# Kernel tuning notes

Measured on AMD Instinct MI355X. Metric: run time of the kernel, lower is better.

Reference implementation:

```python
import jax, jax.numpy as jnp
import numpy as np

B, T, D, H = 512, 200, 128, 128


def setup_inputs() -> dict:
    key = jax.random.key(0)
    ks = jax.random.split(key, 16)
    r = lambda k, shp, s=0.05: jax.random.normal(k, shp, dtype=jnp.float32) * s
    F = 3 * D + H  # concat([item_eb, his_sum, item_eb*his_sum, final_state2])
    return {
        "item_eb": jax.random.normal(ks[0], (B, D), dtype=jnp.float32),
        "item_his_eb": jax.random.normal(ks[1], (B, T, D), dtype=jnp.float32),
        "Wg1": r(ks[2], (D + H, 2 * H)), "bg1": jnp.ones((2 * H,), jnp.float32),
        "Wc1": r(ks[3], (D + H, H)), "bc1": jnp.zeros((H,), jnp.float32),
        "att_w1": r(ks[4], (4 * H, 80)), "att_b1": jnp.zeros((80,), jnp.float32),
        "att_w2": r(ks[5], (80, 40)), "att_b2": jnp.zeros((40,), jnp.float32),
        "att_w3": r(ks[6], (40, 1)), "att_b3": jnp.zeros((1,), jnp.float32),
        "Wg2": r(ks[7], (2 * H, 2 * H)), "bg2": jnp.ones((2 * H,), jnp.float32),
        "Wc2": r(ks[8], (2 * H, H)), "bc2": jnp.zeros((H,), jnp.float32),
        "fc1_w": r(ks[9], (F, 200)), "fc1_b": jnp.zeros((200,), jnp.float32),
        "alpha1": jnp.full((200,), 0.25, jnp.float32),
        "fc2_w": r(ks[10], (200, 80)), "fc2_b": jnp.zeros((80,), jnp.float32),
        "alpha2": jnp.full((80,), 0.25, jnp.float32),
        "fc3_w": r(ks[11], (80, 2)), "fc3_b": jnp.zeros((2,), jnp.float32),
        "seq_len": jax.random.randint(ks[12], (B,), 1, T + 1).astype(jnp.int32),
    }


def _gru_scan(x_btd, Wg, bg, Wc, bc, seq_len, att=None):
    """GRU (TF GRUCell math) or AUGRU if att [B,T] is given.
    Honors sequence_length semantics of tf dynamic_rnn: state copied through,
    outputs zeroed past each row's length."""
    Bx, Tx, _ = x_btd.shape
    Hh = Wc.shape[1]
    xs = jnp.swapaxes(x_btd, 0, 1)  # [T,B,Din]
    ts = jnp.arange(Tx)
    a_ts = jnp.swapaxes(att, 0, 1) if att is not None else jnp.zeros((Tx, Bx), x_btd.dtype)
    h0 = jnp.zeros((Bx, Hh), x_btd.dtype)

    def step(h, xat):
        x, a, t = xat
        gates = jax.nn.sigmoid(jnp.concatenate([x, h], axis=-1) @ Wg + bg)
        rg, u = jnp.split(gates, 2, axis=-1)
        c = jnp.tanh(jnp.concatenate([x, rg * h], axis=-1) @ Wc + bc)
        if att is not None:  # VecAttGRUCell: u = (1 - att_score) * u
            u = (1.0 - a[:, None]) * u
        hn = u * h + (1.0 - u) * c
        valid = (t < seq_len)[:, None]
        hn = jnp.where(valid, hn, h)
        out = jnp.where(valid, hn, jnp.zeros_like(hn))
        return hn, out

    hT, outs = jax.lax.scan(step, h0, (xs, a_ts, ts))
    return jnp.swapaxes(outs, 0, 1), hT  # [B,T,H], [B,H]


def _forward(item_eb, item_his_eb, Wg1, bg1, Wc1, bc1, att_w1, att_b1, att_w2, att_b2,
             att_w3, att_b3, Wg2, bg2, Wc2, bc2, fc1_w, fc1_b, alpha1, fc2_w, fc2_b,
             alpha2, fc3_w, fc3_b, seq_len):
    Bx, Tx, Dx = item_his_eb.shape
    mask = jnp.arange(Tx)[None, :] < seq_len[:, None]  # [B,T] bool
    # rnn_1: plain GRU over history embeddings
    rnn1, _ = _gru_scan(item_his_eb, Wg1, bg1, Wc1, bc1, seq_len)
    # din_fcn_attention: concat trick + 3-layer scorer + masked softmax
    q = jnp.broadcast_to(item_eb[:, None, :], rnn1.shape)
    din_all = jnp.concatenate([q, rnn1, q - rnn1, q * rnn1], axis=-1)  # [B,T,4H]
    h1 = jax.nn.sigmoid(din_all @ att_w1 + att_b1)
    h2 = jax.nn.sigmoid(h1 @ att_w2 + att_b2)
    scores = (h2 @ att_w3 + att_b3)[..., 0]  # [B,T]
    NEG_INF = jnp.float32(-(2.0 ** 32) + 1.0)  # DIEN padding value
    scores = jnp.where(mask, scores, NEG_INF)
    alphas = jax.nn.softmax(scores, axis=-1)  # [B,T]
    # rnn_2: AUGRU (VecAttGRUCell) gated by attention scores; take final state
    _, final_state2 = _gru_scan(rnn1, Wg2, bg2, Wc2, bc2, seq_len, att=alphas)
    # fcn head on concatenated features
    his_sum = jnp.sum(item_his_eb * mask[..., None].astype(item_his_eb.dtype), axis=1)
    feat = jnp.concatenate([item_eb, his_sum, item_eb * his_sum, final_state2], axis=-1)
    prelu = lambda x, a: jnp.maximum(x, 0.0) + a * jnp.minimum(x, 0.0)
    z = prelu(feat @ fc1_w + fc1_b, alpha1)
    z = prelu(z @ fc2_w + fc2_b, alpha2)
    logits = z @ fc3_w + fc3_b  # [B,2]
    return jax.nn.softmax(logits, axis=-1)


def reference(item_eb, item_his_eb, Wg1, bg1, Wc1, bc1, att_w1, att_b1, att_w2, att_b2,
              att_w3, att_b3, Wg2, bg2, Wc2, bc2, fc1_w, fc1_b, alpha1, fc2_w, fc2_b,
              alpha2, fc3_w, fc3_b, seq_len):
    return _forward(item_eb, item_his_eb, Wg1, bg1, Wc1, bc1, att_w1, att_b1, att_w2,
                    att_b2, att_w3, att_b3, Wg2, bg2, Wc2, bc2, fc1_w, fc1_b, alpha1,
                    fc2_w, fc2_b, alpha2, fc3_w, fc3_b, seq_len)
```

## Files before the change

kernel.cpp:

```cpp
#include <hip/hip_runtime.h>
#include <hip/hip_bf16.h>


typedef __attribute__((ext_vector_type(8))) short bf16x8;
typedef __attribute__((ext_vector_type(4))) float f32x4;
typedef _Float16 f16x2 __attribute__((ext_vector_type(2)));

#define NC 4
#define TC 50
#define CROWS 25600
#define CSH 3276800

static __device__ __forceinline__ unsigned short f2bf(float f) {
  union { __hip_bfloat16 h; unsigned short u; } v;
  v.h = __float2bfloat16(f);
  return v.u;
}
static __device__ __forceinline__ float bf2f(unsigned short u) {
  union { __hip_bfloat16 h; unsigned short u; } v;
  v.u = u;
  return __bfloat162float(v.h);
}
static __device__ __forceinline__ unsigned short f2h(float f) {
  union { _Float16 h; unsigned short u; } v;
  v.h = (_Float16)f;
  return v.u;
}
static __device__ __forceinline__ float h2f(unsigned short u) {
  union { unsigned short u; _Float16 h; } v;
  v.u = u;
  return (float)v.h;
}
static __device__ __forceinline__ unsigned int pkf16(float a, float b) {
  union { f16x2 v; unsigned int u; } c;
  c.v = (f16x2){(_Float16)a, (_Float16)b};
  return c.u;
}
static __device__ __forceinline__ void dot2a(float& acc, unsigned int w, unsigned int h) {
  asm volatile("v_dot2_f32_f16 %0, %1, %2, %0" : "+v"(acc) : "v"(w), "v"(h));
}
static __device__ __forceinline__ unsigned short gld_u16(const unsigned short* p) {
  return *(const __attribute__((address_space(1))) unsigned short*)p;
}
static __device__ __forceinline__ float gld_f32(const float* p) {
  return *(const __attribute__((address_space(1))) float*)p;
}
static __device__ __forceinline__ void gst_u16(unsigned short* p, unsigned short v) {
  *(__attribute__((address_space(1))) unsigned short*)p = v;
}
static __device__ __forceinline__ void gst_u32(unsigned int* p, unsigned int v) {
  *(__attribute__((address_space(1))) unsigned int*)p = v;
}
static __device__ __forceinline__ void gst_f32(float* p, float v) {
  *(__attribute__((address_space(1))) float*)p = v;
}
static __device__ __forceinline__ void gbar() {
  __builtin_amdgcn_sched_barrier(0);
  asm volatile("s_waitcnt lgkmcnt(0)" ::: "memory");
  __builtin_amdgcn_s_barrier();
  __builtin_amdgcn_sched_barrier(0);
}

__global__ __launch_bounds__(256) void prep_weights(
    const float* __restrict__ item_eb,
    const float* __restrict__ Wg1, const float* __restrict__ Wc1,
    const float* __restrict__ Wg2, const float* __restrict__ Wc2,
    const float* __restrict__ aw1, const float* __restrict__ aw2,
    const float* __restrict__ aw3,
    const float* __restrict__ bg1, const float* __restrict__ bc1,
    const float* __restrict__ bg2, const float* __restrict__ bc2,
    const float* __restrict__ ab1, const float* __restrict__ ab2,
    unsigned short* __restrict__ W1xT, unsigned short* __restrict__ W2xT,
    unsigned short* __restrict__ AW1T, unsigned short* __restrict__ AW2T,
    float* __restrict__ b384_1, float* __restrict__ b384_2,
    float* __restrict__ bA1, float* __restrict__ bA2,
    unsigned int* __restrict__ WgP1, unsigned int* __restrict__ WcP1,
    unsigned int* __restrict__ WgP2, unsigned int* __restrict__ WcP2,
    float* __restrict__ w3p, unsigned short* __restrict__ Xq,
    float* __restrict__ hstate)
{
  int e = blockIdx.x * 256 + threadIdx.x;
  if (e < 49152) {
    int n = e >> 7, k = e & 127;
    float v1 = (n < 256) ? Wg1[k * 256 + n] : Wc1[k * 128 + (n - 256)];
    float v2 = (n < 256) ? Wg2[k * 256 + n] : Wc2[k * 128 + (n - 256)];
    W1xT[e] = f2bf(v1);
    W2xT[e] = f2bf(v2);
  }
  if (e < 65536) {
    int n = e >> 9, k = e & 511;
    AW1T[e] = f2bf(n < 80 ? aw1[k * 80 + n] : 0.f);
    Xq[e] = f2bf(item_eb[e]);
    hstate[e] = 0.f;
  }
  if (e < 16384) {
    int n = e >> 7, k = e & 127;
    AW2T[e] = f2bf((n < 40 && k < 80) ? aw2[k * 40 + n] : 0.f);
  }
  if (e < 16384) {
    int i = e >> 8, tt = e & 255;
    int row = 128 + 2 * i;
    WgP1[e] = pkf16(Wg1[row * 256 + tt], Wg1[(row + 1) * 256 + tt]);
    WgP2[e] = pkf16(Wg2[row * 256 + tt], Wg2[(row + 1) * 256 + tt]);
  }
  if (e < 8192) {
    int i = e >> 8, tt = e & 255;
    int jc = tt >> 1, half = tt & 1;
    int row = 128 + half * 64 + 2 * i;
    WcP1[e] = pkf16(Wc1[row * 128 + jc], Wc1[(row + 1) * 128 + jc]);
    WcP2[e] = pkf16(Wc2[row * 128 + jc], Wc2[(row + 1) * 128 + jc]);
  }
  if (e < 384) {
    b384_1[e] = (e < 256) ? bg1[e] : bc1[e - 256];
    b384_2[e] = (e < 256) ? bg2[e] : bc2[e - 256];
  }
  if (e < 128) {
    bA1[e] = (e < 80) ? ab1[e] : 0.f;
    bA2[e] = (e < 40) ? ab2[e] : 0.f;
    w3p[e] = (e < 40) ? aw3[e] : 0.f;
  }
}

__global__ __launch_bounds__(256) void cast_his_t(const float4* __restrict__ in4,
                                                  ushort4* __restrict__ out4)
{
  int i = blockIdx.x * 256 + threadIdx.x;
  float4 v = in4[i];
  int d4 = (i & 31) << 2;
  int bt = i >> 5;
  int tt = bt % 200, bb = bt / 200;
  out4[(((size_t)tt * 512 + bb) * 128 + d4) >> 2] =
      make_ushort4(f2bf(v.x), f2bf(v.y), f2bf(v.z), f2bf(v.w));
}

struct GemmP {
  const unsigned short* A;
  const unsigned short* B;
  const float* bias;
  unsigned short* out;
  float* scores;
  const float* w3p;
  const float* b3;
  const unsigned short* Xq;
  const unsigned short* rnn1;
  long rowbase;
  int K, ldc, mtiles, tbase;
};

static __device__ __forceinline__ uint4 bfop(uint4 q, uint4 r, bool mul) {
  unsigned short* qs = (unsigned short*)&q;
  unsigned short* rs = (unsigned short*)&r;
  uint4 o;
  unsigned short* os = (unsigned short*)&o;
#pragma unroll
  for (int i = 0; i < 8; i++) {
    float a = bf2f(qs[i]), b = bf2f(rs[i]);
    os[i] = f2bf(mul ? a * b : a - b);
  }
  return o;
}

template <int SRC, int EPI>
__device__ __forceinline__ void gemm_body(const GemmP& P, int tile, char* smem) {
  uint4* AsB = (uint4*)smem;
  uint4* BsB = AsB + 1024;
  const int tid = threadIdx.x;
  const int w = tid >> 6, l = tid & 63;
  const int mb = tile % P.mtiles, nb = tile / P.mtiles;
  const long mBase = (long)mb * 128;
  const int nBase = nb * 128;

  f32x4 acc[2][8];
#pragma unroll
  for (int m = 0; m < 2; m++)
#pragma unroll
    for (int n = 0; n < 8; n++) acc[m][n] = 0.f;

  const int srow = (tid >> 3) & 31;
  const int scc = l & 7;
  const int KK = SRC ? 512 : P.K;

  for (int kb = 0; kb < KK; kb += 64) {
#pragma unroll
    for (int p = 0; p < 4; p++) {
      int row = p * 32 + srow;
      long grow = mBase + row;
      uint4 va;
      if (SRC == 0) {
        va = *(const uint4*)(P.A + (size_t)grow * KK + kb + scc * 8);
      } else {
        int seg = kb >> 7;
        int c0 = (kb & 127) + scc * 8;
        int b = (int)(grow & 511);
        if (seg == 0) {
          va = *(const uint4*)(P.Xq + b * 128 + c0);
        } else if (seg == 1) {
          va = *(const uint4*)(P.rnn1 + (size_t)(P.rowbase + grow) * 128 + c0);
        } else {
          uint4 vq = *(const uint4*)(P.Xq + b * 128 + c0);
          uint4 vr = *(const uint4*)(P.rnn1 + (size_t)(P.rowbase + grow) * 128 + c0);
          va = bfop(vq, vr, seg == 3);
        }
      }
      uint4 vb = *(const uint4*)(P.B + (size_t)(nBase + row) * KK + kb + scc * 8);
      AsB[row * 8 + (scc ^ (row & 7))] = va;
      BsB[row * 8 + (scc ^ (row & 7))] = vb;
    }
    __syncthreads();
#pragma unroll
    for (int ks = 0; ks < 2; ks++) {
      int ccr = ks * 4 + (l >> 4);
      int r0 = w * 32 + (l & 15);
      int r1 = r0 + 16;
      bf16x8 a0 = *(const bf16x8*)&AsB[r0 * 8 + (ccr ^ (r0 & 7))];
      bf16x8 a1 = *(const bf16x8*)&AsB[r1 * 8 + (ccr ^ (r1 & 7))];
#pragma unroll
      for (int n = 0; n < 8; n++) {
        int rb = n * 16 + (l & 15);
        bf16x8 bn = *(const bf16x8*)&BsB[rb * 8 + (ccr ^ (rb & 7))];
        acc[0][n] = __builtin_amdgcn_mfma_f32_16x16x32_bf16(a0, bn, acc[0][n], 0, 0, 0);
        acc[1][n] = __builtin_amdgcn_mfma_f32_16x16x32_bf16(a1, bn, acc[1][n], 0, 0, 0);
      }
    }
    __syncthreads();
  }

  const int lcol = l & 15, lrow4 = (l >> 4) * 4;
  if (EPI == 2) {
    float sp[2][4] = {{0.f, 0.f, 0.f, 0.f}, {0.f, 0.f, 0.f, 0.f}};
#pragma unroll
    for (int n = 0; n < 8; n++) {
      int gcol = n * 16 + lcol;
      float bb = P.bias[gcol];
      float w3 = P.w3p[gcol];
#pragma unroll
      for (int m = 0; m < 2; m++)
#pragma unroll
        for (int i = 0; i < 4; i++) {
          float v = acc[m][n][i] + bb;
          sp[m][i] += w3 / (1.f + __expf(-v));
        }
    }
#pragma unroll
    for (int msk = 1; msk < 16; msk <<= 1)
#pragma unroll
      for (int m = 0; m < 2; m++)
#pragma unroll
        for (int i = 0; i < 4; i++) sp[m][i] += __shfl_xor(sp[m][i], msk);
    float b3v = P.b3[0];
    if (lcol == 0) {
#pragma unroll
      for (int m = 0; m < 2; m++)
#pragma unroll
        for (int i = 0; i < 4; i++) {
          long grow = mBase + w * 32 + m * 16 + lrow4 + i;
          int b = (int)(grow & 511);
          int tp = (int)(grow >> 9) + P.tbase;
          P.scores[b * 200 + tp] = sp[m][i] + b3v;
        }
    }
  } else {
#pragma unroll
    for (int n = 0; n < 8; n++) {
      int gcol = nBase + n * 16 + lcol;
      float bb = P.bias[gcol];
#pragma unroll
      for (int m = 0; m < 2; m++)
#pragma unroll
        for (int i = 0; i < 4; i++) {
          long grow = mBase + w * 32 + m * 16 + lrow4 + i;
          float v = acc[m][n][i] + bb;
          if (EPI == 0) P.out[grow * P.ldc + gcol] = f2h(v);
          else          P.out[grow * P.ldc + gcol] = f2bf(1.f / (1.f + __expf(-v)));
        }
    }
  }
}

struct GruP {
  const unsigned short* xproj;
  const unsigned int* WgP;
  const unsigned int* WcP;
  const int* seqlen;
  const float* alphas;
  unsigned short* outbf;
  float* hstate;
  int tbase;
};

template <int AUGRU>
static __device__ __forceinline__ void gstep(
    const GruP& P, int r, int t, int jc, int half, int len, int ts, int tsn,
    const unsigned int (&wg)[64], const unsigned int (&wc)[32],
    float* hF, float* uF, unsigned short* hH, unsigned short* rgH,
    unsigned short& gX, unsigned short& cX, float& alX)
{
  const unsigned short* xp = P.xproj;
  const size_t RS = (size_t)512 * 384;
  const size_t base = (size_t)r * 384;
  float xg = h2f(gX), xc = h2f(cX), alv = alX;
  size_t off = (size_t)tsn * RS + base;
  gX = gld_u16(xp + off + t);
  cX = gld_u16(xp + off + 256 + jc);
  if (AUGRU) alX = gld_f32(P.alphas + r * 200 + P.tbase + tsn);

  float a0 = 0.f, a1 = 0.f, a2 = 0.f, a3 = 0.f;
  const uint4* h4 = (const uint4*)hH;
#pragma unroll
  for (int q = 0; q < 4; q++) {
    uint4 h0 = h4[q * 4 + 0];
    uint4 h1 = h4[q * 4 + 1];
    uint4 h2 = h4[q * 4 + 2];
    uint4 h3 = h4[q * 4 + 3];
    dot2a(a0, wg[q * 16 + 0], h0.x);  dot2a(a1, wg[q * 16 + 1], h0.y);
    dot2a(a2, wg[q * 16 + 2], h0.z);  dot2a(a3, wg[q * 16 + 3], h0.w);
    dot2a(a0, wg[q * 16 + 4], h1.x);  dot2a(a1, wg[q * 16 + 5], h1.y);
    dot2a(a2, wg[q * 16 + 6], h1.z);  dot2a(a3, wg[q * 16 + 7], h1.w);
    dot2a(a0, wg[q * 16 + 8], h2.x);  dot2a(a1, wg[q * 16 + 9], h2.y);
    dot2a(a2, wg[q * 16 + 10], h2.z); dot2a(a3, wg[q * 16 + 11], h2.w);
    dot2a(a0, wg[q * 16 + 12], h3.x); dot2a(a1, wg[q * 16 + 13], h3.y);
    dot2a(a2, wg[q * 16 + 14], h3.z); dot2a(a3, wg[q * 16 + 15], h3.w);
  }
  float a = (a0 + a1) + (a2 + a3) + xg;
  float g = 1.f / (1.f + __expf(-a));
  if (t < 128) rgH[t] = f2h(g * hF[t]);
  else         uF[t - 128] = g;
  gbar();

  float c0 = 0.f, c1 = 0.f;
  const uint4* rp = (const uint4*)rgH + half * 8;
#pragma unroll
  for (int q = 0; q < 8; q++) {
    uint4 rq = rp[q];
    dot2a(c0, wc[q * 4 + 0], rq.x);
    dot2a(c1, wc[q * 4 + 1], rq.y);
    dot2a(c0, wc[q * 4 + 2], rq.z);
    dot2a(c1, wc[q * 4 + 3], rq.w);
  }
  float c = c0 + c1;
  c += __shfl_xor(c, 1);
  c += xc;
  c = fminf(fmaxf(c, -15.f), 15.f);
  float e2 = __expf(2.f * c);
  c = 1.f - 2.f / (e2 + 1.f);
  float u = uF[jc];
  if (AUGRU) u *= (1.f - alv);
  float h = hF[jc];
  float hn = u * h + (1.f - u) * c;
  bool valid = (P.tbase + ts) < len;
  hn = valid ? hn : h;
  if (!half) {
    hF[jc] = hn;
    hH[jc] = f2h(hn);
    if (!AUGRU)
      gst_u16(P.outbf + ((size_t)(P.tbase + ts) * 512 + r) * 128 + jc,
              valid ? f2bf(hn) : (unsigned short)0);
  }
  gbar();
}

template <int AUGRU>
__device__ void gru_body(const GruP& P, int r, char* smem) {
  float* hF = (float*)smem;
  float* uF = hF + 128;
  unsigned short* hH = (unsigned short*)(uF + 128);
  unsigned short* rgH = hH + 128;
  const int t = threadIdx.x;
  const int jc = t >> 1, half = t & 1;
  const int len = P.seqlen[r];
  int nsteps = len - P.tbase;
  if (nsteps > TC) nsteps = TC;

  if (nsteps <= 0) {
    if (!AUGRU && t < 64) {
      for (int s = 0; s < TC; s++)
        gst_u32((unsigned int*)(P.outbf + ((size_t)(P.tbase + s) * 512 + r) * 128) + t, 0u);
    }
    return;
  }
  __builtin_amdgcn_s_setprio(1);

  unsigned int wg[64], wc[32];
#pragma unroll
  for (int i = 0; i < 64; i++) wg[i] = P.WgP[i * 256 + t];
#pragma unroll
  for (int i = 0; i < 32; i++) wc[i] = P.WcP[i * 256 + t];

  if (t < 128) {
    float h = gld_f32(P.hstate + r * 128 + t);
    hF[t] = h;
    hH[t] = f2h(h);
  }
  gbar();

  const unsigned short* xp = P.xproj;
  const size_t RS = (size_t)512 * 384;
  const size_t base = (size_t)r * 384;
  unsigned short gE = gld_u16(xp + base + t), cE = gld_u16(xp + base + 256 + jc);
  int s1 = nsteps > 1 ? 1 : 0;
  unsigned short gO = gld_u16(xp + s1 * RS + base + t);
  unsigned short cO = gld_u16(xp + s1 * RS + base + 256 + jc);
  float alE = AUGRU ? gld_f32(P.alphas + r * 200 + P.tbase) : 0.f;
  float alO = AUGRU ? gld_f32(P.alphas + r * 200 + P.tbase + s1) : 0.f;

  int rsteps = (nsteps + 1) & ~1;
  for (int ts = 0; ts < rsteps; ts += 2) {
    int tn0 = (ts + 2 < nsteps) ? ts + 2 : nsteps - 1;
    int tn1 = (ts + 3 < nsteps) ? ts + 3 : nsteps - 1;
    gstep<AUGRU>(P, r, t, jc, half, len, ts,     tn0, wg, wc, hF, uF, hH, rgH, gE, cE, alE);
    gstep<AUGRU>(P, r, t, jc, half, len, ts + 1, tn1, wg, wc, hF, uF, hH, rgH, gO, cO, alO);
  }

  if (t < 128) gst_f32(P.hstate + r * 128 + t, hF[t]);
  if (!AUGRU && t < 64) {
    for (int s = rsteps; s < TC; s++)
      gst_u32((unsigned int*)(P.outbf + ((size_t)(P.tbase + s) * 512 + r) * 128) + t, 0u);
  }
}

__device__ void hsum_body(const float* __restrict__ his, float* __restrict__ hs,
                          const int* __restrict__ seqlen, int b, char* smem) {
  float* sm = (float*)smem;
  int t = threadIdx.x;
  int len = seqlen[b];
  int col = t & 127, hf = t >> 7;
  float s = 0.f;
  for (int ts = hf; ts < len; ts += 2) s += his[((size_t)b * 200 + ts) * 128 + col];
  sm[t] = s;
  __syncthreads();
  if (t < 128) hs[b * 128 + t] = sm[t] + sm[t + 128];
}

template <int AUG, int GRU, int S1, int E1, int S2, int E2, int S3, int E3, int HS>
__global__ __launch_bounds__(256) void fatk(GruP gp, GemmP p1, int c1,
                                            GemmP p2, int c2, GemmP p3,
                                            const float* hisp, float* hsp)
{
  extern __shared__ char smem[];
  int id = blockIdx.x;
  if constexpr (GRU) {
    if (id < 512) { gru_body<AUG>(gp, id, smem); return; }
    id -= 512;
  }
  if constexpr (HS) {
    if (id < 512) { hsum_body(hisp, hsp, gp.seqlen, id, smem); return; }
    id -= 512;
  }
  if constexpr (S1 >= 0) {
    if (id < c1) { gemm_body<S1, E1>(p1, id, smem); return; }
    id -= c1;
  }
  if constexpr (S2 >= 0) {
    if (id < c2) { gemm_body<S2, E2>(p2, id, smem); return; }
    id -= c2;
  }
  if constexpr (S3 >= 0) gemm_body<S3, E3>(p3, id, smem);
}

__global__ __launch_bounds__(256) void mask_softmax(
    const float* __restrict__ scores, const int* __restrict__ seqlen,
    float* __restrict__ alphas, float* __restrict__ hstate)
{
  int b = blockIdx.x, t = threadIdx.x;
  __shared__ float red[256];
  if (t < 128) hstate[b * 128 + t] = 0.f;
  int len = seqlen[b];
  float s = (t < 200 && t < len) ? scores[b * 200 + t] : -1e30f;
  red[t] = s;
  __syncthreads();
  for (int o = 128; o > 0; o >>= 1) {
    if (t < o) red[t] = fmaxf(red[t], red[t + o]);
    __syncthreads();
  }
  float m = red[0];
  __syncthreads();
  float e = (t < 200 && t < len) ? __expf(s - m) : 0.f;
  red[t] = e;
  __syncthreads();
  for (int o = 128; o > 0; o >>= 1) {
    if (t < o) red[t] += red[t + o];
    __syncthreads();
  }
  float denom = red[0];
  if (t < 200) alphas[b * 200 + t] = e / denom;
}

__global__ __launch_bounds__(256) void head_kernel(
    const float* __restrict__ item_eb, const float* __restrict__ hs,
    const float* __restrict__ hstate,
    const float* __restrict__ w1, const float* __restrict__ b1, const float* __restrict__ a1,
    const float* __restrict__ w2, const float* __restrict__ b2, const float* __restrict__ a2,
    const float* __restrict__ w3, const float* __restrict__ b3,
    float* __restrict__ out)
{
  int b = blockIdx.x, t = threadIdx.x;
  __shared__ float frow[512];
  __shared__ float z1[200];
  __shared__ float z2[80];
  if (t < 128) {
    float sv = hs[b * 128 + t];
    float q = item_eb[b * 128 + t];
    frow[t] = q;
    frow[128 + t] = sv;
    frow[256 + t] = q * sv;
    frow[384 + t] = hstate[b * 128 + t];
  }
  __syncthreads();
  if (t < 200) {
    float acc = b1[t];
#pragma unroll 8
    for (int k = 0; k < 512; k++) acc += frow[k] * w1[k * 200 + t];
    z1[t] = acc > 0.f ? acc : a1[t] * acc;
  }
  __syncthreads();
  if (t < 80) {
    float acc = b2[t];
#pragma unroll 8
    for (int k = 0; k < 200; k++) acc += z1[k] * w2[k * 80 + t];
    z2[t] = acc > 0.f ? acc : a2[t] * acc;
  }
  __syncthreads();
  if (t == 0) {
    float l0 = b3[0], l1 = b3[1];
    for (int k = 0; k < 80; k++) {
      float z = z2[k];
      l0 += z * w3[k * 2];
      l1 += z * w3[k * 2 + 1];
    }
    float m = fmaxf(l0, l1);
    float e0 = __expf(l0 - m), e1 = __expf(l1 - m);
    out[b * 2 + 0] = e0 / (e0 + e1);
    out[b * 2 + 1] = e1 / (e0 + e1);
  }
}

extern "C" void kernel_launch(void* const* d_in, const int* in_sizes, int n_in,
                              void* d_out, int out_size, void* d_ws, size_t ws_size,
                              hipStream_t stream)
{
  const float* item_eb = (const float*)d_in[0];
  const float* his     = (const float*)d_in[1];
  const float* Wg1     = (const float*)d_in[2];
  const float* bg1     = (const float*)d_in[3];
  const float* Wc1     = (const float*)d_in[4];
  const float* bc1     = (const float*)d_in[5];
  const float* aw1     = (const float*)d_in[6];
  const float* ab1     = (const float*)d_in[7];
  const float* aw2     = (const float*)d_in[8];
  const float* ab2     = (const float*)d_in[9];
  const float* aw3     = (const float*)d_in[10];
  const float* ab3     = (const float*)d_in[11];
  const float* Wg2     = (const float*)d_in[12];
  const float* bg2     = (const float*)d_in[13];
  const float* Wc2     = (const float*)d_in[14];
  const float* bc2     = (const float*)d_in[15];
  const float* fc1w    = (const float*)d_in[16];
  const float* fc1b    = (const float*)d_in[17];
  const float* al1     = (const float*)d_in[18];
  const float* fc2w    = (const float*)d_in[19];
  const float* fc2b    = (const float*)d_in[20];
  const float* al2     = (const float*)d_in[21];
  const float* fc3w    = (const float*)d_in[22];
  const float* fc3b    = (const float*)d_in[23];
  const int*   seqlen  = (const int*)d_in[24];

  char* ws = (char*)d_ws;
  unsigned short* XhA    = (unsigned short*)(ws + 0L);
  unsigned short* xpA    = (unsigned short*)(ws + 26214400L);
  unsigned short* xpB    = (unsigned short*)(ws + 45875200L);
  unsigned short* rnn1   = (unsigned short*)(ws + 65536000L);
  float*          scores = (float*)(ws + 91750400L);
  float*          alphas = (float*)(ws + 92160000L);
  float*          hstate = (float*)(ws + 92569600L);
  unsigned int*   WgP1   = (unsigned int*)(ws + 92831744L);
  unsigned int*   WcP1   = (unsigned int*)(ws + 92897280L);
  unsigned int*   WgP2   = (unsigned int*)(ws + 92930048L);
  unsigned int*   WcP2   = (unsigned int*)(ws + 92995584L);
  unsigned short* W1xT   = (unsigned short*)(ws + 93028352L);
  unsigned short* W2xT   = (unsigned short*)(ws + 93126656L);
  unsigned short* AW1T   = (unsigned short*)(ws + 93224960L);
  unsigned short* AW2T   = (unsigned short*)(ws + 93356032L);
  float*          b384_1 = (float*)(ws + 93388800L);
  float*          b384_2 = (float*)(ws + 93390336L);
  float*          bA1    = (float*)(ws + 93391872L);
  float*          bA2    = (float*)(ws + 93392384L);
  float*          w3p    = (float*)(ws + 93392896L);
  unsigned short* Xq     = (unsigned short*)(ws + 93393408L);
  float*          hs     = scores;

  unsigned short* h1[NC] = {XhA, XhA + CSH, XhA + 2 * CSH, XhA + 3 * CSH};

  const int SM = 32768;
  GruP gz{}; GemmP dz{};
  gz.seqlen = seqlen;

  auto mkGru = [&](int c, int aug) {
    GruP g;
    g.xproj = (c & 1) ? xpB : xpA;
    g.WgP = aug ? WgP2 : WgP1; g.WcP = aug ? WcP2 : WcP1;
    g.seqlen = seqlen; g.alphas = alphas;
    g.outbf = aug ? nullptr : rnn1; g.hstate = hstate; g.tbase = c * TC;
    return g;
  };
  auto mkXp = [&](const unsigned short* A, const float* bias, unsigned short* outp) {
    GemmP p{}; p.A = A; p.B = (bias == b384_1) ? W1xT : W2xT; p.bias = bias;
    p.out = outp; p.K = 128; p.ldc = 384; p.mtiles = 200; return p;
  };
  auto mkAtt1 = [&](int c) {
    GemmP p{}; p.B = AW1T; p.bias = bA1; p.out = h1[c];
    p.Xq = Xq; p.rnn1 = rnn1; p.rowbase = (long)c * CROWS;
    p.K = 512; p.ldc = 128; p.mtiles = 200; return p;
  };
  auto mkAtt2 = [&](int c) {
    GemmP p{}; p.A = h1[c]; p.B = AW2T; p.bias = bA2;
    p.scores = scores; p.w3p = w3p; p.b3 = ab3;
    p.K = 128; p.ldc = 128; p.mtiles = 200; p.tbase = c * TC; return p;
  };

  prep_weights<<<256, 256, 0, stream>>>(item_eb, Wg1, Wc1, Wg2, Wc2, aw1, aw2, aw3,
                                        bg1, bc1, bg2, bc2, ab1, ab2,
                                        W1xT, W2xT, AW1T, AW2T, b384_1, b384_2, bA1, bA2,
                                        WgP1, WcP1, WgP2, WcP2, w3p, Xq, hstate);
  cast_his_t<<<12800, 256, 0, stream>>>((const float4*)his, (ushort4*)XhA);

  fatk<0,0, 0,0, -1,0, -1,0, 0><<<600, 256, SM, stream>>>(
      gz, mkXp(XhA, b384_1, xpA), 600, dz, 0, dz, nullptr, nullptr);
  fatk<0,1, 0,0, -1,0, -1,0, 0><<<1112, 256, SM, stream>>>(
      mkGru(0,0), mkXp(XhA + (size_t)CSH, b384_1, xpB), 600, dz, 0, dz, nullptr, nullptr);
  fatk<0,1, 0,0, -1,0, -1,0, 0><<<1112, 256, SM, stream>>>(
      mkGru(1,0), mkXp(XhA + (size_t)2*CSH, b384_1, xpA), 600, dz, 0, dz, nullptr, nullptr);
  fatk<0,1, 0,0, 1,1, -1,0, 0><<<1712, 256, SM, stream>>>(
      mkGru(2,0), mkXp(XhA + (size_t)3*CSH, b384_1, xpB), 600, mkAtt1(0), 200, dz, nullptr, nullptr);
  fatk<0,1, 1,1, 0,2, -1,0, 0><<<912, 256, SM, stream>>>(
      mkGru(3,0), mkAtt1(1), 200, mkAtt2(0), 200, dz, nullptr, nullptr);
  fatk<0,0, 1,1, 0,2, 0,0, 0><<<1000, 256, SM, stream>>>(
      gz, mkAtt1(2), 200, mkAtt2(1), 200, mkXp(rnn1, b384_2, xpA), nullptr, nullptr);
  fatk<0,0, 1,1, 0,2, 0,0, 0><<<1000, 256, SM, stream>>>(
      gz, mkAtt1(3), 200, mkAtt2(2), 200, mkXp(rnn1 + (size_t)CSH, b384_2, xpB), nullptr, nullptr);
  fatk<0,0, 0,2, -1,0, -1,0, 0><<<200, 256, SM, stream>>>(
      gz, mkAtt2(3), 200, dz, 0, dz, nullptr, nullptr);
  mask_softmax<<<512, 256, 0, stream>>>(scores, seqlen, alphas, hstate);
  fatk<1,1, -1,0, -1,0, -1,0, 1><<<1024, 256, SM, stream>>>(
      mkGru(0,1), dz, 0, dz, 0, dz, his, hs);
  fatk<1,1, 0,0, -1,0, -1,0, 0><<<1112, 256, SM, stream>>>(
      mkGru(1,1), mkXp(rnn1 + (size_t)2*CSH, b384_2, xpA), 600, dz, 0, dz, nullptr, nullptr);
  fatk<1,1, 0,0, -1,0, -1,0, 0><<<1112, 256, SM, stream>>>(
      mkGru(2,1), mkXp(rnn1 + (size_t)3*CSH, b384_2, xpB), 600, dz, 0, dz, nullptr, nullptr);
  fatk<1,1, -1,0, -1,0, -1,0, 0><<<512, 256, SM, stream>>>(
      mkGru(3,1), dz, 0, dz, 0, dz, nullptr, nullptr);
  head_kernel<<<512, 256, 0, stream>>>(item_eb, hs, hstate,
                                       fc1w, fc1b, al1, fc2w, fc2b, al2,
                                       fc3w, fc3b, (float*)d_out);
}
```

Measured before the change: 646.0 us.

## Remap GRU recurrence so 128 threads each own one hidden unit

The recurrent GRU step is restructured so that each of 128 active threads computes both the reset and update gate and the full candidate dot product for one hidden unit, keeping h in a register. The fp32 LDS state copies, the split-K shuffle reduction and half the LDS traffic are removed, and the weight packing is re-laid out into separate reset, update and candidate arrays. Threads 128-255 now only take part in the barriers and return. Each active thread holds 192 packed weight registers instead of 96, and per-step serial work per thread doubles, which could raise latency on the critical recurrent path or cause register spills.

Result: slower. 948.1 us (+46.8%).

```diff
diff --git a/kernel.cpp b/kernel.cpp
--- a/kernel.cpp
+++ b/kernel.cpp
@@ -74,8 +74,10 @@
     unsigned short* __restrict__ AW1T, unsigned short* __restrict__ AW2T,
     float* __restrict__ b384_1, float* __restrict__ b384_2,
     float* __restrict__ bA1, float* __restrict__ bA2,
-    unsigned int* __restrict__ WgP1, unsigned int* __restrict__ WcP1,
-    unsigned int* __restrict__ WgP2, unsigned int* __restrict__ WcP2,
+    unsigned int* __restrict__ WgrP1, unsigned int* __restrict__ WguP1,
+    unsigned int* __restrict__ WcP1,
+    unsigned int* __restrict__ WgrP2, unsigned int* __restrict__ WguP2,
+    unsigned int* __restrict__ WcP2,
     float* __restrict__ w3p, unsigned short* __restrict__ Xq,
     float* __restrict__ hstate)
 {
@@ -97,18 +99,15 @@
     int n = e >> 7, k = e & 127;
     AW2T[e] = f2bf((n < 40 && k < 80) ? aw2[k * 40 + n] : 0.f);
   }
-  if (e < 16384) {
-    int i = e >> 8, tt = e & 255;
+  if (e < 8192) {
+    int i = e >> 7, tt = e & 127;
     int row = 128 + 2 * i;
-    WgP1[e] = pkf16(Wg1[row * 256 + tt], Wg1[(row + 1) * 256 + tt]);
-    WgP2[e] = pkf16(Wg2[row * 256 + tt], Wg2[(row + 1) * 256 + tt]);
-  }
-  if (e < 8192) {
-    int i = e >> 8, tt = e & 255;
-    int jc = tt >> 1, half = tt & 1;
-    int row = 128 + half * 64 + 2 * i;
-    WcP1[e] = pkf16(Wc1[row * 128 + jc], Wc1[(row + 1) * 128 + jc]);
-    WcP2[e] = pkf16(Wc2[row * 128 + jc], Wc2[(row + 1) * 128 + jc]);
+    WgrP1[e] = pkf16(Wg1[row * 256 + tt],       Wg1[(row + 1) * 256 + tt]);
+    WguP1[e] = pkf16(Wg1[row * 256 + 128 + tt], Wg1[(row + 1) * 256 + 128 + tt]);
+    WcP1[e]  = pkf16(Wc1[row * 128 + tt],       Wc1[(row + 1) * 128 + tt]);
+    WgrP2[e] = pkf16(Wg2[row * 256 + tt],       Wg2[(row + 1) * 256 + tt]);
+    WguP2[e] = pkf16(Wg2[row * 256 + 128 + tt], Wg2[(row + 1) * 256 + 128 + tt]);
+    WcP2[e]  = pkf16(Wc2[row * 128 + tt],       Wc2[(row + 1) * 128 + tt]);
   }
   if (e < 384) {
     b384_1[e] = (e < 256) ? bg1[e] : bc1[e - 256];
@@ -279,8 +278,9 @@
 
 struct GruP {
   const unsigned short* xproj;
-  const unsigned int* WgP;
-  const unsigned int* WcP;
+  const unsigned int* Wgr;
+  const unsigned int* Wgu;
+  const unsigned int* Wc;
   const int* seqlen;
   const float* alphas;
   unsigned short* outbf;
@@ -290,83 +290,101 @@
 
 template <int AUGRU>
 static __device__ __forceinline__ void gstep(
-    const GruP& P, int r, int t, int jc, int half, int len, int ts, int tsn,
-    const unsigned int (&wg)[64], const unsigned int (&wc)[32],
-    float* hF, float* uF, unsigned short* hH, unsigned short* rgH,
-    unsigned short& gX, unsigned short& cX, float& alX)
+    const GruP& P, int r, int t, int len, int ts, int tsn,
+    const unsigned int (&wgr)[64], const unsigned int (&wgu)[64],
+    const unsigned int (&wcv)[64],
+    unsigned short* hH, unsigned short* rgH,
+    unsigned short& gR, unsigned short& gU, unsigned short& cX, float& alX,
+    float& h)
 {
   const unsigned short* xp = P.xproj;
   const size_t RS = (size_t)512 * 384;
   const size_t base = (size_t)r * 384;
-  float xg = h2f(gX), xc = h2f(cX), alv = alX;
+  float xr = h2f(gR), xu = h2f(gU), xc = h2f(cX), alv = alX;
   size_t off = (size_t)tsn * RS + base;
-  gX = gld_u16(xp + off + t);
-  cX = gld_u16(xp + off + 256 + jc);
+  gR = gld_u16(xp + off + t);
+  gU = gld_u16(xp + off + 128 + t);
+  cX = gld_u16(xp + off + 256 + t);
   if (AUGRU) alX = gld_f32(P.alphas + r * 200 + P.tbase + tsn);
 
   float a0 = 0.f, a1 = 0.f, a2 = 0.f, a3 = 0.f;
+  float b0 = 0.f, b1 = 0.f, b2 = 0.f, b3 = 0.f;
   const uint4* h4 = (const uint4*)hH;
 #pragma unroll
   for (int q = 0; q < 4; q++) {
-    uint4 h0 = h4[q * 4 + 0];
-    uint4 h1 = h4[q * 4 + 1];
-    uint4 h2 = h4[q * 4 + 2];
-    uint4 h3 = h4[q * 4 + 3];
-    dot2a(a0, wg[q * 16 + 0], h0.x);  dot2a(a1, wg[q * 16 + 1], h0.y);
-    dot2a(a2, wg[q * 16 + 2], h0.z);  dot2a(a3, wg[q * 16 + 3], h0.w);
-    dot2a(a0, wg[q * 16 + 4], h1.x);  dot2a(a1, wg[q * 16 + 5], h1.y);
-    dot2a(a2, wg[q * 16 + 6], h1.z);  dot2a(a3, wg[q * 16 + 7], h1.w);
-    dot2a(a0, wg[q * 16 + 8], h2.x);  dot2a(a1, wg[q * 16 + 9], h2.y);
-    dot2a(a2, wg[q * 16 + 10], h2.z); dot2a(a3, wg[q * 16 + 11], h2.w);
-    dot2a(a0, wg[q * 16 + 12], h3.x); dot2a(a1, wg[q * 16 + 13], h3.y);
-    dot2a(a2, wg[q * 16 + 14], h3.z); dot2a(a3, wg[q * 16 + 15], h3.w);
-  }
-  float a = (a0 + a1) + (a2 + a3) + xg;
-  float g = 1.f / (1.f + __expf(-a));
-  if (t < 128) rgH[t] = f2h(g * hF[t]);
-  else         uF[t - 128] = g;
+    uint4 u0 = h4[q * 4 + 0];
+    uint4 u1 = h4[q * 4 + 1];
+    uint4 u2 = h4[q * 4 + 2];
+    uint4 u3 = h4[q * 4 + 3];
+    dot2a(a0, wgr[q * 16 + 0], u0.x);  dot2a(b0, wgu[q * 16 + 0], u0.x);
+    dot2a(a1, wgr[q * 16 + 1], u0.y);  dot2a(b1, wgu[q * 16 + 1], u0.y);
+    dot2a(a2, wgr[q * 16 + 2], u0.z);  dot2a(b2, wgu[q * 16 + 2], u0.z);
+    dot2a(a3, wgr[q * 16 + 3], u0.w);  dot2a(b3, wgu[q * 16 + 3], u0.w);
+    dot2a(a0, wgr[q * 16 + 4], u1.x);  dot2a(b0, wgu[q * 16 + 4], u1.x);
+    dot2a(a1, wgr[q * 16 + 5], u1.y);  dot2a(b1, wgu[q * 16 + 5], u1.y);
+    dot2a(a2, wgr[q * 16 + 6], u1.z);  dot2a(b2, wgu[q * 16 + 6], u1.z);
+    dot2a(a3, wgr[q * 16 + 7], u1.w);  dot2a(b3, wgu[q * 16 + 7], u1.w);
+    dot2a(a0, wgr[q * 16 + 8], u2.x);  dot2a(b0, wgu[q * 16 + 8], u2.x);
+    dot2a(a1, wgr[q * 16 + 9], u2.y);  dot2a(b1, wgu[q * 16 + 9], u2.y);
+    dot2a(a2, wgr[q * 16 + 10], u2.z); dot2a(b2, wgu[q * 16 + 10], u2.z);
+    dot2a(a3, wgr[q * 16 + 11], u2.w); dot2a(b3, wgu[q * 16 + 11], u2.w);
+    dot2a(a0, wgr[q * 16 + 12], u3.x); dot2a(b0, wgu[q * 16 + 12], u3.x);
+    dot2a(a1, wgr[q * 16 + 13], u3.y); dot2a(b1, wgu[q * 16 + 13], u3.y);
+    dot2a(a2, wgr[q * 16 + 14], u3.z); dot2a(b2, wgu[q * 16 + 14], u3.z);
+    dot2a(a3, wgr[q * 16 + 15], u3.w); dot2a(b3, wgu[q * 16 + 15], u3.w);
+  }
+  float ar = (a0 + a1) + (a2 + a3) + xr;
+  float au = (b0 + b1) + (b2 + b3) + xu;
+  float rg = 1.f / (1.f + __expf(-ar));
+  float ug = 1.f / (1.f + __expf(-au));
+  rgH[t] = f2h(rg * h);
   gbar();
 
-  float c0 = 0.f, c1 = 0.f;
-  const uint4* rp = (const uint4*)rgH + half * 8;
-#pragma unroll
-  for (int q = 0; q < 8; q++) {
-    uint4 rq = rp[q];
-    dot2a(c0, wc[q * 4 + 0], rq.x);
-    dot2a(c1, wc[q * 4 + 1], rq.y);
-    dot2a(c0, wc[q * 4 + 2], rq.z);
-    dot2a(c1, wc[q * 4 + 3], rq.w);
-  }
-  float c = c0 + c1;
-  c += __shfl_xor(c, 1);
-  c += xc;
+  float c0 = 0.f, c1 = 0.f, c2 = 0.f, c3 = 0.f;
+  const uint4* r4 = (const uint4*)rgH;
+#pragma unroll
+  for (int q = 0; q < 4; q++) {
+    uint4 u0 = r4[q * 4 + 0];
+    uint4 u1 = r4[q * 4 + 1];
+    uint4 u2 = r4[q * 4 + 2];
+    uint4 u3 = r4[q * 4 + 3];
+    dot2a(c0, wcv[q * 16 + 0], u0.x);
+    dot2a(c1, wcv[q * 16 + 1], u0.y);
+    dot2a(c2, wcv[q * 16 + 2], u0.z);
+    dot2a(c3, wcv[q * 16 + 3], u0.w);
+    dot2a(c0, wcv[q * 16 + 4], u1.x);
+    dot2a(c1, wcv[q * 16 + 5], u1.y);
+    dot2a(c2, wcv[q * 16 + 6], u1.z);
+    dot2a(c3, wcv[q * 16 + 7], u1.w);
+    dot2a(c0, wcv[q * 16 + 8], u2.x);
+    dot2a(c1, wcv[q * 16 + 9], u2.y);
+    dot2a(c2, wcv[q * 16 + 10], u2.z);
+    dot2a(c3, wcv[q * 16 + 11], u2.w);
+    dot2a(c0, wcv[q * 16 + 12], u3.x);
+    dot2a(c1, wcv[q * 16 + 13], u3.y);
+    dot2a(c2, wcv[q * 16 + 14], u3.z);
+    dot2a(c3, wcv[q * 16 + 15], u3.w);
+  }
+  float c = (c0 + c1) + (c2 + c3) + xc;
   c = fminf(fmaxf(c, -15.f), 15.f);
   float e2 = __expf(2.f * c);
   c = 1.f - 2.f / (e2 + 1.f);
-  float u = uF[jc];
-  if (AUGRU) u *= (1.f - alv);
-  float h = hF[jc];
-  float hn = u * h + (1.f - u) * c;
+  float ue = AUGRU ? ug * (1.f - alv) : ug;
+  float hn = ue * h + (1.f - ue) * c;
   bool valid = (P.tbase + ts) < len;
-  hn = valid ? hn : h;
-  if (!half) {
-    hF[jc] = hn;
-    hH[jc] = f2h(hn);
-    if (!AUGRU)
-      gst_u16(P.outbf + ((size_t)(P.tbase + ts) * 512 + r) * 128 + jc,
-              valid ? f2bf(hn) : (unsigned short)0);
-  }
+  h = valid ? hn : h;
+  hH[t] = f2h(h);
+  if (!AUGRU)
+    gst_u16(P.outbf + ((size_t)(P.tbase + ts) * 512 + r) * 128 + t,
+            valid ? f2bf(h) : (unsigned short)0);
   gbar();
 }
 
 template <int AUGRU>
 __device__ void gru_body(const GruP& P, int r, char* smem) {
-  float* hF = (float*)smem;
-  float* uF = hF + 128;
-  unsigned short* hH = (unsigned short*)(uF + 128);
+  unsigned short* hH = (unsigned short*)smem;
   unsigned short* rgH = hH + 128;
   const int t = threadIdx.x;
-  const int jc = t >> 1, half = t & 1;
   const int len = P.seqlen[r];
   int nsteps = len - P.tbase;
   if (nsteps > TC) nsteps = TC;
@@ -378,40 +396,48 @@
     }
     return;
   }
+  int rsteps = (nsteps + 1) & ~1;
+
+  if (t >= 128) {
+    gbar();
+    for (int s = 0; s < rsteps; s++) { gbar(); gbar(); }
+    return;
+  }
   __builtin_amdgcn_s_setprio(1);
 
-  unsigned int wg[64], wc[32];
-#pragma unroll
-  for (int i = 0; i < 64; i++) wg[i] = P.WgP[i * 256 + t];
-#pragma unroll
-  for (int i = 0; i < 32; i++) wc[i] = P.WcP[i * 256 + t];
-
-  if (t < 128) {
-    float h = gld_f32(P.hstate + r * 128 + t);
-    hF[t] = h;
-    hH[t] = f2h(h);
-  }
+  unsigned int wgr[64], wgu[64], wcv[64];
+#pragma unroll
+  for (int i = 0; i < 64; i++) wgr[i] = P.Wgr[i * 128 + t];
+#pragma unroll
+  for (int i = 0; i < 64; i++) wgu[i] = P.Wgu[i * 128 + t];
+#pragma unroll
+  for (int i = 0; i < 64; i++) wcv[i] = P.Wc[i * 128 + t];
+
+  float h = gld_f32(P.hstate + r * 128 + t);
+  hH[t] = f2h(h);
   gbar();
 
   const unsigned short* xp = P.xproj;
   const size_t RS = (size_t)512 * 384;
   const size_t base = (size_t)r * 384;
-  unsigned short gE = gld_u16(xp + base + t), cE = gld_u16(xp + base + 256 + jc);
+  unsigned short gRE = gld_u16(xp + base + t);
+  unsigned short gUE = gld_u16(xp + base + 128 + t);
+  unsigned short cXE = gld_u16(xp + base + 256 + t);
   int s1 = nsteps > 1 ? 1 : 0;
-  unsigned short gO = gld_u16(xp + s1 * RS + base + t);
-  unsigned short cO = gld_u16(xp + s1 * RS + base + 256 + jc);
+  unsigned short gRO = gld_u16(xp + s1 * RS + base + t);
+  unsigned short gUO = gld_u16(xp + s1 * RS + base + 128 + t);
+  unsigned short cXO = gld_u16(xp + s1 * RS + base + 256 + t);
   float alE = AUGRU ? gld_f32(P.alphas + r * 200 + P.tbase) : 0.f;
   float alO = AUGRU ? gld_f32(P.alphas + r * 200 + P.tbase + s1) : 0.f;
 
-  int rsteps = (nsteps + 1) & ~1;
   for (int ts = 0; ts < rsteps; ts += 2) {
     int tn0 = (ts + 2 < nsteps) ? ts + 2 : nsteps - 1;
     int tn1 = (ts + 3 < nsteps) ? ts + 3 : nsteps - 1;
-    gstep<AUGRU>(P, r, t, jc, half, len, ts,     tn0, wg, wc, hF, uF, hH, rgH, gE, cE, alE);
-    gstep<AUGRU>(P, r, t, jc, half, len, ts + 1, tn1, wg, wc, hF, uF, hH, rgH, gO, cO, alO);
-  }
-
-  if (t < 128) gst_f32(P.hstate + r * 128 + t, hF[t]);
+    gstep<AUGRU>(P, r, t, len, ts,     tn0, wgr, wgu, wcv, hH, rgH, gRE, gUE, cXE, alE, h);
+    gstep<AUGRU>(P, r, t, len, ts + 1, tn1, wgr, wgu, wcv, hH, rgH, gRO, gUO, cXO, alO, h);
+  }
+
+  gst_f32(P.hstate + r * 128 + t, h);
   if (!AUGRU && t < 64) {
     for (int s = rsteps; s < TC; s++)
       gst_u32((unsigned int*)(P.outbf + ((size_t)(P.tbase + s) * 512 + r) * 128) + t, 0u);
@@ -572,9 +598,11 @@
   float*          scores = (float*)(ws + 91750400L);
   float*          alphas = (float*)(ws + 92160000L);
   float*          hstate = (float*)(ws + 92569600L);
-  unsigned int*   WgP1   = (unsigned int*)(ws + 92831744L);
+  unsigned int*   WgrP1  = (unsigned int*)(ws + 92831744L);
+  unsigned int*   WguP1  = (unsigned int*)(ws + 92864512L);
   unsigned int*   WcP1   = (unsigned int*)(ws + 92897280L);
-  unsigned int*   WgP2   = (unsigned int*)(ws + 92930048L);
+  unsigned int*   WgrP2  = (unsigned int*)(ws + 92930048L);
+  unsigned int*   WguP2  = (unsigned int*)(ws + 92962816L);
   unsigned int*   WcP2   = (unsigned int*)(ws + 92995584L);
   unsigned short* W1xT   = (unsigned short*)(ws + 93028352L);
   unsigned short* W2xT   = (unsigned short*)(ws + 93126656L);
@@ -597,7 +625,9 @@
   auto mkGru = [&](int c, int aug) {
     GruP g;
     g.xproj = (c & 1) ? xpB : xpA;
-    g.WgP = aug ? WgP2 : WgP1; g.WcP = aug ? WcP2 : WcP1;
+    g.Wgr = aug ? WgrP2 : WgrP1;
+    g.Wgu = aug ? WguP2 : WguP1;
+    g.Wc  = aug ? WcP2  : WcP1;
     g.seqlen = seqlen; g.alphas = alphas;
     g.outbf = aug ? nullptr : rnn1; g.hstate = hstate; g.tbase = c * TC;
     return g;
@@ -620,7 +650,8 @@
   prep_weights<<<256, 256, 0, stream>>>(item_eb, Wg1, Wc1, Wg2, Wc2, aw1, aw2, aw3,
                                         bg1, bc1, bg2, bc2, ab1, ab2,
                                         W1xT, W2xT, AW1T, AW2T, b384_1, b384_2, bA1, bA2,
-                                        WgP1, WcP1, WgP2, WcP2, w3p, Xq, hstate);
+                                        WgrP1, WguP1, WcP1, WgrP2, WguP2, WcP2,
+                                        w3p, Xq, hstate);
   cast_his_t<<<12800, 256, 0, stream>>>((const float4*)his, (ushort4*)XhA);
 
   fatk<0,0, 0,0, -1,0, -1,0, 0><<<600, 256, SM, stream>>>(
```
